# Kernel optimization log

Measured on AMD Instinct MI355X. Metric: run time of the kernel, lower is better.

## Reference

```python
import jax, jax.numpy as jnp
import numpy as np

N_NODES, N_EDGES, D_IN, D_OUT = 50000, 800000, 64, 64
N_REL, N_TIME = 500, 1000


def setup_inputs() -> dict:
    key = jax.random.key(0)
    ks = jax.random.split(key, 14)
    xavier = lambda k, shape: jax.random.normal(k, shape, jnp.float32) * np.sqrt(2.0 / (shape[0] + shape[1])) * np.sqrt(2.0)
    return {
        "x": jax.random.normal(ks[0], (N_NODES, D_IN), jnp.float32),
        "rel_repr": jax.random.normal(ks[1], (N_REL, D_IN), jnp.float32),
        "time_emds": jax.random.normal(ks[2], (N_TIME, D_IN), jnp.float32),
        "src": jax.random.randint(ks[3], (N_EDGES,), 0, N_NODES),
        "dst": jax.random.randint(ks[4], (N_EDGES,), 0, N_NODES),
        "etype": jax.random.randint(ks[5], (N_EDGES,), 0, N_REL),
        "etime": jax.random.randint(ks[6], (N_EDGES,), 0, N_TIME),
        "trans_w": xavier(ks[7], (D_IN, D_OUT)),
        "loop_w": xavier(ks[8], (D_IN, D_OUT)),
        "w_rel": xavier(ks[9], (D_IN, D_OUT)),
        "attn_h": xavier(ks[10], (D_IN, 1)),
        "attn_t": xavier(ks[11], (D_IN, 1)),
        "attn_r": xavier(ks[12], (D_IN, 1)),
        "attn_ts": xavier(ks[13], (D_IN, 1)),
    }


def reference(x, rel_repr, time_emds, src, dst, etype, etime,
              trans_w, loop_w, w_rel, attn_h, attn_t, attn_r, attn_ts):
    n = x.shape[0]
    # per-node / per-rel / per-time scalar attention projections
    h_att = (x @ attn_h)[:, 0]          # [N]
    t_att = (x @ attn_t)[:, 0]          # [N]
    r_att = (rel_repr @ attn_r)[:, 0]   # [R]
    ts_att = (time_emds @ attn_ts)[:, 0]  # [T]
    # edge attention logits + edge_softmax grouped by destination node
    e = jax.nn.leaky_relu(h_att[src] - t_att[dst] + r_att[etype] + ts_att[etime], 0.1)  # [E]
    m = jax.ops.segment_max(e, dst, num_segments=n)
    ex = jnp.exp(e - m[dst])
    den = jax.ops.segment_sum(ex, dst, num_segments=n)
    att = (ex / den[dst])[:, None]      # [E,1]
    # message: (head + time) * (rel + time) -> trans_w -> weighted scatter-sum to dst
    time_emd = time_emds[etime]         # [E,D]
    edge_data = (x[src] + time_emd) * (rel_repr[etype] + time_emd)
    msg = (edge_data @ trans_w) * att   # [E,D_out]
    h = jax.ops.segment_sum(msg, dst, num_segments=n)
    x_out = h + x @ loop_w
    rel_out = rel_repr @ w_rel
    return (x_out, rel_out)
```

## Files before the change

kernel.cpp:

```cpp
#include <hip/hip_runtime.h>
#include <hip/hip_bf16.h>

#define N_NODES 50000
#define N_EDGES 800000
#define D 64
#define N_REL 500
#define N_TIME 1000
#define SLOTS 64
#define NODE_BLOCKS ((N_NODES + 63) / 64)
#define REL_BLOCKS  ((N_REL + 63) / 64)

#define CB 64
#define NCB ((N_NODES + CB - 1) / CB)
#define FR 64
#define NFB ((N_NODES + FR - 1) / FR)
#define SCAP 2048
#define BINCAP 8
#define BTILE 4096
#define LSLOT 48

__device__ __forceinline__ float bf2f(unsigned short u) {
    union { unsigned int i; float f; } v;
    v.i = ((unsigned int)u) << 16;
    return v.f;
}

__global__ void proj_kernel(const float* __restrict__ x,
                            const float* __restrict__ rel,
                            const float* __restrict__ tim,
                            const float* __restrict__ ah,
                            const float* __restrict__ at,
                            const float* __restrict__ ar,
                            const float* __restrict__ ats,
                            float* __restrict__ h_att, float* __restrict__ t_att,
                            float* __restrict__ r_att, float* __restrict__ ts_att,
                            unsigned short* __restrict__ x_bf,
                            int* __restrict__ cursor) {
    int gid = blockIdx.x * blockDim.x + threadIdx.x;
    if (gid < NCB) cursor[gid] = 0;
    int wave = gid >> 6;
    int lane = threadIdx.x & 63;
    const int total = N_NODES + N_REL + N_TIME;
    if (wave >= total) return;
    if (wave < N_NODES) {
        float xv = x[wave * D + lane];
        __hip_bfloat16 b = __float2bfloat16(xv);
        x_bf[wave * D + lane] = *(unsigned short*)&b;
        float s1 = xv * ah[lane];
        float s2 = xv * at[lane];
        for (int off = 32; off; off >>= 1) {
            s1 += __shfl_down(s1, off);
            s2 += __shfl_down(s2, off);
        }
        if (lane == 0) { h_att[wave] = s1; t_att[wave] = s2; }
    } else if (wave < N_NODES + N_REL) {
        int r = wave - N_NODES;
        float v = rel[r * D + lane] * ar[lane];
        for (int off = 32; off; off >>= 1) v += __shfl_down(v, off);
        if (lane == 0) r_att[r] = v;
    } else {
        int t = wave - N_NODES - N_REL;
        float v = tim[t * D + lane] * ats[lane];
        for (int off = 32; off; off >>= 1) v += __shfl_down(v, off);
        if (lane == 0) ts_att[t] = v;
    }
}

__global__ __launch_bounds__(512)
void bin_kernel(const int* __restrict__ src, const int* __restrict__ dst,
                const int* __restrict__ etype, const int* __restrict__ etime,
                const float* __restrict__ h_att, const float* __restrict__ t_att,
                const float* __restrict__ r_att, const float* __restrict__ ts_att,
                int* __restrict__ cursor, int4* __restrict__ stage) {
    __shared__ int4 bins[NCB][BINCAP];
    __shared__ int bcnt[NCB];
    int t = threadIdx.x;
    for (int k = t; k < NCB; k += 512) bcnt[k] = 0;
    __syncthreads();

    int e0 = blockIdx.x * BTILE;
    for (int j = 0; j < 8; j++) {
        int e = e0 + j * 512 + t;
        if (e < N_EDGES) {
            int s = src[e], d = dst[e], r = etype[e], tt = etime[e];
            float lg = h_att[s] - t_att[d] + r_att[r] + ts_att[tt];
            float lr = lg > 0.f ? lg : 0.1f * lg;
            float ex = __expf(lr);
            unsigned exb = __float_as_uint(ex);
            int4 rec;
            rec.x = (int)((exb & ~7u) | (unsigned)(s & 7));
            rec.y = (int)(((unsigned)(s >> 3) << 19) | ((unsigned)r << 10) | (unsigned)tt);
            rec.z = d;
            rec.w = 0;
            int k = d >> 6;
            int pos = atomicAdd(&bcnt[k], 1);
            if (pos < BINCAP) {
                bins[k][pos] = rec;
            } else {
                int g = atomicAdd(&cursor[k], 1);
                if (g < SCAP) stage[(size_t)k * SCAP + g] = rec;
            }
        }
    }
    __syncthreads();
    for (int k = t; k < NCB; k += 512) {
        int c = bcnt[k];
        if (c > BINCAP) c = BINCAP;
        if (c > 0) {
            int base = atomicAdd(&cursor[k], c);
            for (int i = 0; i < c; i++) {
                int g = base + i;
                if (g < SCAP) stage[(size_t)k * SCAP + g] = bins[k][i];
            }
        }
    }
}

__global__ __launch_bounds__(512)
void node_fused_kernel(const unsigned short* __restrict__ x_bf,
                       const float* __restrict__ rel,
                       const float* __restrict__ tim,
                       const float* __restrict__ x,
                       const float* __restrict__ trans_w,
                       const float* __restrict__ loop_w,
                       const int* __restrict__ cursor,
                       const int4* __restrict__ stage,
                       float* __restrict__ out) {
    __shared__ char  uni[FR * LSLOT * 8];
    __shared__ int   lcnt[FR];
    __shared__ float Wt[D * D];
    __shared__ float Wl[D * D];
    __shared__ float Xt[FR * D];
    int2*  lslot = (int2*)uni;
    float* At    = (float*)uni;

    int tid = threadIdx.x;
    int base = blockIdx.x * FR;
    int pb = blockIdx.x;

    for (int i = tid; i < FR; i += 512) lcnt[i] = 0;
    for (int j = 0; j < 2; j++) {
        int idx = (tid + 512 * j) * 4;
        *(float4*)(Wt + idx) = *(const float4*)(trans_w + idx);
        *(float4*)(Wl + idx) = *(const float4*)(loop_w + idx);
    }
    for (int j = 0; j < 2; j++) {
        int lin = tid + 512 * j;
        int rr = lin >> 4;
        int k4 = (lin & 15) << 2;
        int gr = base + rr; if (gr >= N_NODES) gr = N_NODES - 1;
        *(float4*)(Xt + rr * D + k4) = *(const float4*)(x + (size_t)gr * D + k4);
    }
    __syncthreads();

    int n = cursor[pb];
    if (n > SCAP) n = SCAP;
    for (int i = tid; i < n; i += 512) {
        int4 rec = stage[(size_t)pb * SCAP + i];
        int ln = rec.z - base;
        if ((unsigned)ln < FR) {
            int pos = atomicAdd(&lcnt[ln], 1);
            if (pos < LSLOT) lslot[ln * LSLOT + pos] = make_int2(rec.x, rec.y);
        }
    }
    __syncthreads();

    int lane = tid & 63;
    int wv = tid >> 6;
    int qw = lane >> 4;
    int ql = lane & 15;
    float4 acc4[8];

#pragma unroll
    for (int j = 0; j < 8; j++) {
        int ln = wv + j * 8;
        int deg = lcnt[ln];
        if (deg > LSLOT) deg = LSLOT;

        int s_l = 0, r_l = 0, t_l = 0;
        float ex = 0.f;
        if (lane < deg) {
            int2 pl = lslot[ln * LSLOT + lane];
            unsigned px = (unsigned)pl.x;
            unsigned py = (unsigned)pl.y;
            ex = __uint_as_float(px & ~7u);
            s_l = (int)(((py >> 19) << 3) | (px & 7u));
            r_l = (int)((py >> 10) & 511u);
            t_l = (int)(py & 1023u);
        }
        float den = ex;
        for (int off = 32; off; off >>= 1) den += __shfl_xor(den, off);
        float att_l = (lane < deg) ? ex / den : 0.f;

        float4 acc = make_float4(0.f, 0.f, 0.f, 0.f);
        for (int i = 0; i < deg; i += 8) {
            int eiA = i + qw;
            int eiB = i + 4 + qw;
            int sA = __shfl(s_l, eiA), rA = __shfl(r_l, eiA), tA = __shfl(t_l, eiA);
            float attA = __shfl(att_l, eiA);
            int sB = __shfl(s_l, eiB), rB = __shfl(r_l, eiB), tB = __shfl(t_l, eiB);
            float attB = __shfl(att_l, eiB);
            float4  teA = *(const float4*)(tim + tA * D + ql * 4);
            ushort4 xbA = *(const ushort4*)(x_bf + sA * D + ql * 4);
            float4  rlA = *(const float4*)(rel + rA * D + ql * 4);
            float4  teB = *(const float4*)(tim + tB * D + ql * 4);
            ushort4 xbB = *(const ushort4*)(x_bf + sB * D + ql * 4);
            float4  rlB = *(const float4*)(rel + rB * D + ql * 4);
            acc.x += attA * (bf2f(xbA.x) + teA.x) * (rlA.x + teA.x);
            acc.y += attA * (bf2f(xbA.y) + teA.y) * (rlA.y + teA.y);
            acc.z += attA * (bf2f(xbA.z) + teA.z) * (rlA.z + teA.z);
            acc.w += attA * (bf2f(xbA.w) + teA.w) * (rlA.w + teA.w);
            acc.x += attB * (bf2f(xbB.x) + teB.x) * (rlB.x + teB.x);
            acc.y += attB * (bf2f(xbB.y) + teB.y) * (rlB.y + teB.y);
            acc.z += attB * (bf2f(xbB.z) + teB.z) * (rlB.z + teB.z);
            acc.w += attB * (bf2f(xbB.w) + teB.w) * (rlB.w + teB.w);
        }
        for (int off = 16; off <= 32; off <<= 1) {
            acc.x += __shfl_xor(acc.x, off);
            acc.y += __shfl_xor(acc.y, off);
            acc.z += __shfl_xor(acc.z, off);
            acc.w += __shfl_xor(acc.w, off);
        }
        acc4[j] = acc;
    }
    __syncthreads();

#pragma unroll
    for (int j = 0; j < 8; j++) {
        if (qw == 0) {
            int ln = wv + j * 8;
            *(float4*)(At + ln * D + ql * 4) = acc4[j];
        }
    }
    __syncthreads();

    int c4 = ql << 2;
    int r0 = wv * 8 + qw * 2;
    float acc[2][4];
    for (int i = 0; i < 2; i++)
        for (int c = 0; c < 4; c++) acc[i][c] = 0.f;

    for (int k = 0; k < D; k += 4) {
        float wt[4][4], wl[4][4];
        for (int kk = 0; kk < 4; kk++) {
            *(float4*)&wt[kk][0] = *(const float4*)(Wt + (k + kk) * D + c4);
            *(float4*)&wl[kk][0] = *(const float4*)(Wl + (k + kk) * D + c4);
        }
        for (int i = 0; i < 2; i++) {
            float a[4], xv[4];
            *(float4*)&a[0]  = *(const float4*)(At + (r0 + i) * D + k);
            *(float4*)&xv[0] = *(const float4*)(Xt + (r0 + i) * D + k);
            for (int c = 0; c < 4; c++) {
                float s = acc[i][c];
                for (int kk = 0; kk < 4; kk++)
                    s += a[kk] * wt[kk][c] + xv[kk] * wl[kk][c];
                acc[i][c] = s;
            }
        }
    }
    for (int i = 0; i < 2; i++) {
        int gr = base + r0 + i;
        if (gr < N_NODES)
            *(float4*)(out + (size_t)gr * D + c4) = *(float4*)&acc[i][0];
    }
}

__global__ __launch_bounds__(256)
void rel_gemm_kernel(const float* __restrict__ rel,
                     const float* __restrict__ w_rel,
                     float* __restrict__ out) {
    __shared__ float Wa[D * D];
    __shared__ float At[64 * D];
    int t = threadIdx.x;
    int row0 = blockIdx.x * 64;

    for (int j = 0; j < 4; j++) {
        int idx = (t + 256 * j) * 4;
        *(float4*)(Wa + idx) = *(const float4*)(w_rel + idx);
    }
    for (int j = 0; j < 4; j++) {
        int lin = t + 256 * j;
        int rr = lin >> 4;
        int k4 = (lin & 15) << 2;
        int gr = row0 + rr; if (gr >= N_REL) gr = N_REL - 1;
        *(float4*)(At + rr * D + k4) = *(const float4*)(rel + (size_t)gr * D + k4);
    }
    __syncthreads();

    int lane = t & 63;
    int wv = t >> 6;
    int c4 = (lane & 15) << 2;
    int r0 = wv * 16 + (lane >> 4) * 4;

    float acc[4][4];
    for (int i = 0; i < 4; i++)
        for (int c = 0; c < 4; c++) acc[i][c] = 0.f;

    for (int k = 0; k < D; k += 4) {
        float wt[4][4];
        for (int kk = 0; kk < 4; kk++)
            *(float4*)&wt[kk][0] = *(const float4*)(Wa + (k + kk) * D + c4);
        for (int i = 0; i < 4; i++) {
            float a[4];
            *(float4*)&a[0] = *(const float4*)(At + (r0 + i) * D + k);
            for (int c = 0; c < 4; c++) {
                float s = acc[i][c];
                for (int kk = 0; kk < 4; kk++)
                    s += a[kk] * wt[kk][c];
                acc[i][c] = s;
            }
        }
    }
    for (int i = 0; i < 4; i++) {
        int gr = row0 + r0 + i;
        if (gr < N_REL)
            *(float4*)(out + (size_t)(N_NODES + gr) * D + c4) = *(float4*)&acc[i][0];
    }
}

__global__ void build_kernel(const int* __restrict__ src, const int* __restrict__ dst,
                             const int* __restrict__ etype, const int* __restrict__ etime,
                             const float* __restrict__ h_att, const float* __restrict__ t_att,
                             const float* __restrict__ r_att, const float* __restrict__ ts_att,
                             int* __restrict__ cnt, int2* __restrict__ payload) {
    int e = blockIdx.x * blockDim.x + threadIdx.x;
    if (e >= N_EDGES) return;
    int s = src[e], d = dst[e], r = etype[e], t = etime[e];
    float lg = h_att[s] - t_att[d] + r_att[r] + ts_att[t];
    float lr = lg > 0.f ? lg : 0.1f * lg;
    float ex = __expf(lr);
    unsigned exb = __float_as_uint(ex);
    int2 pl;
    pl.x = (int)((exb & ~7u) | (unsigned)(s & 7));
    pl.y = (int)(((unsigned)(s >> 3) << 19) | ((unsigned)r << 10) | (unsigned)t);
    int pos = atomicAdd(&cnt[d], 1);
    if (pos < SLOTS) payload[(d << 6) + pos] = pl;
}

__global__ void node_gather_kernel(const unsigned short* __restrict__ x_bf,
                                   const float* __restrict__ rel,
                                   const float* __restrict__ tim,
                                   const int* __restrict__ cnt,
                                   const int2* __restrict__ payload,
                                   float* __restrict__ agg) {
    int d = (blockIdx.x * blockDim.x + threadIdx.x) >> 6;
    int lane = threadIdx.x & 63;
    if (d >= N_NODES) return;
    int deg = cnt[d];
    if (deg > SLOTS) deg = SLOTS;
    int s_l = 0, r_l = 0, t_l = 0;
    float ex = 0.f;
    if (lane < deg) {
        int2 pl = payload[(d << 6) + lane];
        unsigned px = (unsigned)pl.x;
        unsigned py = (unsigned)pl.y;
        ex = __uint_as_float(px & ~7u);
        s_l = (int)(((py >> 19) << 3) | (px & 7u));
        r_l = (int)((py >> 10) & 511u);
        t_l = (int)(py & 1023u);
    }
    float den = ex;
    for (int off = 32; off; off >>= 1) den += __shfl_xor(den, off);
    float att_l = (lane < deg) ? ex / den : 0.f;
    int qw = lane >> 4;
    int ql = lane & 15;
    float4 acc = make_float4(0.f, 0.f, 0.f, 0.f);
    for (int i = 0; i < deg; i += 4) {
        int ei = i + qw;
        int s = __shfl(s_l, ei);
        int r = __shfl(r_l, ei);
        int t = __shfl(t_l, ei);
        float att = __shfl(att_l, ei);
        float4  te = *(const float4*)(tim + t * D + ql * 4);
        ushort4 xb = *(const ushort4*)(x_bf + s * D + ql * 4);
        float4  rl = *(const float4*)(rel + r * D + ql * 4);
        acc.x += att * (bf2f(xb.x) + te.x) * (rl.x + te.x);
        acc.y += att * (bf2f(xb.y) + te.y) * (rl.y + te.y);
        acc.z += att * (bf2f(xb.z) + te.z) * (rl.z + te.z);
        acc.w += att * (bf2f(xb.w) + te.w) * (rl.w + te.w);
    }
    for (int off = 16; off <= 32; off <<= 1) {
        acc.x += __shfl_xor(acc.x, off);
        acc.y += __shfl_xor(acc.y, off);
        acc.z += __shfl_xor(acc.z, off);
        acc.w += __shfl_xor(acc.w, off);
    }
    if (qw == 0)
        *(float4*)(agg + (d << 7) + ql * 4) = acc;
}

__global__ __launch_bounds__(256, 2)
void out_gemm_kernel(const float* __restrict__ agg,
                     const float* __restrict__ x,
                     const float* __restrict__ rel,
                     const float* __restrict__ trans_w,
                     const float* __restrict__ loop_w,
                     const float* __restrict__ w_rel,
                     float* __restrict__ out, int astride) {
    __shared__ float Wa[D * D];
    __shared__ float Wb[D * D];
    __shared__ float At[64 * D];
    __shared__ float Xt[64 * D];
    int t = threadIdx.x;
    bool nodeb = blockIdx.x < NODE_BLOCKS;
    int row0 = nodeb ? blockIdx.x * 64 : (blockIdx.x - NODE_BLOCKS) * 64;

    for (int j = 0; j < 4; j++) {
        int idx = (t + 256 * j) * 4;
        if (nodeb) {
            *(float4*)(Wa + idx) = *(const float4*)(trans_w + idx);
            *(float4*)(Wb + idx) = *(const float4*)(loop_w + idx);
        } else {
            *(float4*)(Wa + idx) = *(const float4*)(w_rel + idx);
        }
    }
    for (int j = 0; j < 4; j++) {
        int lin = t + 256 * j;
        int rr = lin >> 4;
        int k4 = (lin & 15) << 2;
        if (nodeb) {
            int gr = row0 + rr; if (gr >= N_NODES) gr = N_NODES - 1;
            *(float4*)(At + rr * D + k4) = *(const float4*)(agg + (size_t)gr * astride + k4);
            *(float4*)(Xt + rr * D + k4) = *(const float4*)(x + (size_t)gr * D + k4);
        } else {
            int gr = row0 + rr; if (gr >= N_REL) gr = N_REL - 1;
            *(float4*)(At + rr * D + k4) = *(const float4*)(rel + (size_t)gr * D + k4);
        }
    }
    __syncthreads();

    int lane = t & 63;
    int wv = t >> 6;
    int c4 = (lane & 15) << 2;
    int r0 = wv * 16 + (lane >> 4) * 4;

    float acc[4][4];
    for (int i = 0; i < 4; i++)
        for (int c = 0; c < 4; c++) acc[i][c] = 0.f;

    if (nodeb) {
        for (int k = 0; k < D; k += 4) {
            float wt[4][4], wl[4][4];
            for (int kk = 0; kk < 4; kk++) {
                *(float4*)&wt[kk][0] = *(const float4*)(Wa + (k + kk) * D + c4);
                *(float4*)&wl[kk][0] = *(const float4*)(Wb + (k + kk) * D + c4);
            }
            for (int i = 0; i < 4; i++) {
                float a[4], xv[4];
                *(float4*)&a[0]  = *(const float4*)(At + (r0 + i) * D + k);
                *(float4*)&xv[0] = *(const float4*)(Xt + (r0 + i) * D + k);
                for (int c = 0; c < 4; c++) {
                    float s = acc[i][c];
                    for (int kk = 0; kk < 4; kk++)
                        s += a[kk] * wt[kk][c] + xv[kk] * wl[kk][c];
                    acc[i][c] = s;
                }
            }
        }
        for (int i = 0; i < 4; i++) {
            int gr = row0 + r0 + i;
            if (gr < N_NODES)
                *(float4*)(out + (size_t)gr * D + c4) = *(float4*)&acc[i][0];
        }
    } else {
        for (int k = 0; k < D; k += 4) {
            float wt[4][4];
            for (int kk = 0; kk < 4; kk++)
                *(float4*)&wt[kk][0] = *(const float4*)(Wa + (k + kk) * D + c4);
            for (int i = 0; i < 4; i++) {
                float a[4];
                *(float4*)&a[0] = *(const float4*)(At + (r0 + i) * D + k);
                for (int c = 0; c < 4; c++) {
                    float s = acc[i][c];
                    for (int kk = 0; kk < 4; kk++)
                        s += a[kk] * wt[kk][c];
                    acc[i][c] = s;
                }
            }
        }
        for (int i = 0; i < 4; i++) {
            int gr = row0 + r0 + i;
            if (gr < N_REL)
                *(float4*)(out + (size_t)(N_NODES + gr) * D + c4) = *(float4*)&acc[i][0];
        }
    }
}

extern "C" void kernel_launch(void* const* d_in, const int* in_sizes, int n_in,
                              void* d_out, int out_size, void* d_ws, size_t ws_size,
                              hipStream_t stream) {
    const float* x    = (const float*)d_in[0];
    const float* rel  = (const float*)d_in[1];
    const float* tim  = (const float*)d_in[2];
    const int* src   = (const int*)d_in[3];
    const int* dst   = (const int*)d_in[4];
    const int* etype = (const int*)d_in[5];
    const int* etime = (const int*)d_in[6];
    const float* trans_w = (const float*)d_in[7];
    const float* loop_w  = (const float*)d_in[8];
    const float* w_rel   = (const float*)d_in[9];
    const float* ah  = (const float*)d_in[10];
    const float* at  = (const float*)d_in[11];
    const float* ar  = (const float*)d_in[12];
    const float* ats = (const float*)d_in[13];

    char* ws = (char*)d_ws;
    int*   cursor         = (int*)  (ws);
    int*   cnt            = (int*)  (ws);
    float* h_att          = (float*)(ws + 200064);
    float* t_att          = (float*)(ws + 400064);
    float* r_att          = (float*)(ws + 600064);
    float* ts_att         = (float*)(ws + 602064);
    float* agg            = (float*)(ws + 1000000);
    int2*  payload        = (int2*) (ws + 1000000);
    unsigned short* x_bf  = (unsigned short*)(ws + 26600000);
    int4*  stage          = (int4*) (ws + 33000000);

    float* out = (float*)d_out;

    const size_t need = 33000000ull + (size_t)NCB * SCAP * sizeof(int4);
    const bool fused = (ws_size >= need);

    if (!fused)
        hipMemsetAsync(cnt, 0, 200000, stream);

    {
        int waves = N_NODES + N_REL + N_TIME;
        proj_kernel<<<(waves + 3) / 4, 256, 0, stream>>>(
            x, rel, tim, ah, at, ar, ats,
            h_att, t_att, r_att, ts_att, x_bf, cursor);
    }
    if (fused) {
        bin_kernel<<<(N_EDGES + BTILE - 1) / BTILE, 512, 0, stream>>>(
            src, dst, etype, etime, h_att, t_att, r_att, ts_att,
            cursor, stage);
        node_fused_kernel<<<NFB, 512, 0, stream>>>(
            x_bf, rel, tim, x, trans_w, loop_w, cursor, stage, out);
        rel_gemm_kernel<<<REL_BLOCKS, 256, 0, stream>>>(rel, w_rel, out);
    } else {
        build_kernel<<<(N_EDGES + 255) / 256, 256, 0, stream>>>(
            src, dst, etype, etime, h_att, t_att, r_att, ts_att, cnt, payload);
        node_gather_kernel<<<(N_NODES + 3) / 4, 256, 0, stream>>>(
            x_bf, rel, tim, cnt, payload, agg);
        out_gemm_kernel<<<NODE_BLOCKS + REL_BLOCKS, 256, 0, stream>>>(
            agg, x, rel, trans_w, loop_w, w_rel, out, 128);
    }
}
```

Baseline: 187.3 us.

## Shrink node kernel LDS footprint to raise occupancy, read edges directly from LDS

```diff
diff --git a/kernel.cpp b/kernel.cpp
--- a/kernel.cpp
+++ b/kernel.cpp
@@ -17,7 +17,7 @@
 #define SCAP 2048
 #define BINCAP 8
 #define BTILE 4096
-#define LSLOT 48
+#define LSLOT 40
 
 __device__ __forceinline__ float bf2f(unsigned short u) {
     union { unsigned int i; float f; } v;
@@ -116,7 +116,7 @@
     }
 }
 
-__global__ __launch_bounds__(512)
+__global__ __launch_bounds__(512, 6)
 void node_fused_kernel(const unsigned short* __restrict__ x_bf,
                        const float* __restrict__ rel,
                        const float* __restrict__ tim,
@@ -126,30 +126,25 @@
                        const int* __restrict__ cursor,
                        const int4* __restrict__ stage,
                        float* __restrict__ out) {
-    __shared__ char  uni[FR * LSLOT * 8];
+    __shared__ int2  lslot_s[FR * LSLOT];
     __shared__ int   lcnt[FR];
     __shared__ float Wt[D * D];
     __shared__ float Wl[D * D];
-    __shared__ float Xt[FR * D];
-    int2*  lslot = (int2*)uni;
-    float* At    = (float*)uni;
+    float* At = (float*)lslot_s;
 
     int tid = threadIdx.x;
     int base = blockIdx.x * FR;
     int pb = blockIdx.x;
 
     for (int i = tid; i < FR; i += 512) lcnt[i] = 0;
+    {
+        int2 z = make_int2(0, 0);
+        for (int i = tid; i < FR * LSLOT; i += 512) lslot_s[i] = z;
+    }
     for (int j = 0; j < 2; j++) {
         int idx = (tid + 512 * j) * 4;
         *(float4*)(Wt + idx) = *(const float4*)(trans_w + idx);
         *(float4*)(Wl + idx) = *(const float4*)(loop_w + idx);
-    }
-    for (int j = 0; j < 2; j++) {
-        int lin = tid + 512 * j;
-        int rr = lin >> 4;
-        int k4 = (lin & 15) << 2;
-        int gr = base + rr; if (gr >= N_NODES) gr = N_NODES - 1;
-        *(float4*)(Xt + rr * D + k4) = *(const float4*)(x + (size_t)gr * D + k4);
     }
     __syncthreads();
 
@@ -160,7 +155,7 @@
         int ln = rec.z - base;
         if ((unsigned)ln < FR) {
             int pos = atomicAdd(&lcnt[ln], 1);
-            if (pos < LSLOT) lslot[ln * LSLOT + pos] = make_int2(rec.x, rec.y);
+            if (pos < LSLOT) lslot_s[ln * LSLOT + pos] = make_int2(rec.x, rec.y);
         }
     }
     __syncthreads();
@@ -177,29 +172,32 @@
         int deg = lcnt[ln];
         if (deg > LSLOT) deg = LSLOT;
 
-        int s_l = 0, r_l = 0, t_l = 0;
         float ex = 0.f;
         if (lane < deg) {
-            int2 pl = lslot[ln * LSLOT + lane];
-            unsigned px = (unsigned)pl.x;
-            unsigned py = (unsigned)pl.y;
-            ex = __uint_as_float(px & ~7u);
-            s_l = (int)(((py >> 19) << 3) | (px & 7u));
-            r_l = (int)((py >> 10) & 511u);
-            t_l = (int)(py & 1023u);
+            int2 pl = lslot_s[ln * LSLOT + lane];
+            ex = __uint_as_float((unsigned)pl.x & ~7u);
         }
         float den = ex;
         for (int off = 32; off; off >>= 1) den += __shfl_xor(den, off);
-        float att_l = (lane < deg) ? ex / den : 0.f;
-
+        float rden = 1.f / den;
+
+        const int2* row = lslot_s + ln * LSLOT;
         float4 acc = make_float4(0.f, 0.f, 0.f, 0.f);
         for (int i = 0; i < deg; i += 8) {
-            int eiA = i + qw;
-            int eiB = i + 4 + qw;
-            int sA = __shfl(s_l, eiA), rA = __shfl(r_l, eiA), tA = __shfl(t_l, eiA);
-            float attA = __shfl(att_l, eiA);
-            int sB = __shfl(s_l, eiB), rB = __shfl(r_l, eiB), tB = __shfl(t_l, eiB);
-            float attB = __shfl(att_l, eiB);
+            int eA = i + qw;
+            int eB = i + 4 + qw;
+            int2 pA = row[eA];
+            int2 pB = row[eB];
+            unsigned pxA = (unsigned)pA.x, pyA = (unsigned)pA.y;
+            unsigned pxB = (unsigned)pB.x, pyB = (unsigned)pB.y;
+            float attA = (eA < deg) ? __uint_as_float(pxA & ~7u) * rden : 0.f;
+            float attB = (eB < deg) ? __uint_as_float(pxB & ~7u) * rden : 0.f;
+            int sA = (int)(((pyA >> 19) << 3) | (pxA & 7u));
+            int rA = (int)((pyA >> 10) & 511u);
+            int tA = (int)(pyA & 1023u);
+            int sB = (int)(((pyB >> 19) << 3) | (pxB & 7u));
+            int rB = (int)((pyB >> 10) & 511u);
+            int tB = (int)(pyB & 1023u);
             float4  teA = *(const float4*)(tim + tA * D + ql * 4);
             ushort4 xbA = *(const ushort4*)(x_bf + sA * D + ql * 4);
             float4  rlA = *(const float4*)(rel + rA * D + ql * 4);
@@ -247,9 +245,11 @@
             *(float4*)&wl[kk][0] = *(const float4*)(Wl + (k + kk) * D + c4);
         }
         for (int i = 0; i < 2; i++) {
+            int gr = base + r0 + i;
+            int grc = gr < N_NODES ? gr : N_NODES - 1;
             float a[4], xv[4];
             *(float4*)&a[0]  = *(const float4*)(At + (r0 + i) * D + k);
-            *(float4*)&xv[0] = *(const float4*)(Xt + (r0 + i) * D + k);
+            *(float4*)&xv[0] = *(const float4*)(x + (size_t)grc * D + k);
             for (int c = 0; c < 4; c++) {
                 float s = acc[i][c];
                 for (int kk = 0; kk < 4; kk++)
```

Measured after the change: 201.3 us. 7.5% more time.
